# Kernel tuning notes

Hardware: AMD Instinct MI355X
Metric: run time of the kernel (lower is better)

The kernel has to match this reference:

```python
import jax, jax.numpy as jnp
import numpy as np

BZ, T, D, DFF, E, BEAMS = 128, 32, 768, 3072, 8, 2


def setup_inputs() -> dict:
    key = jax.random.key(0)
    ks = jax.random.split(key, 4)
    s = 0.02
    return {
        "x": jax.random.normal(ks[0], (BZ, T, D), jnp.float32),
        "attention_mask": jnp.ones((BZ, T), jnp.float32),
        "Wg": jax.random.normal(ks[1], (D, E), jnp.float32) * s,   # gate Linear(D,E,bias=False)
        "W1": jax.random.normal(ks[2], (E, D, DFF), jnp.float32) * s,
        "b1": jnp.zeros((E, DFF), jnp.float32),
        "W2": jax.random.normal(ks[3], (E, DFF, D), jnp.float32) * s,
        "b2": jnp.zeros((E, D), jnp.float32),
    }


def reference(x, attention_mask, Wg, W1, b1, W2, b2):
    # forward_gate: module builds its own all-ones mask regardless of input mask
    mask = jnp.ones((x.shape[0], x.shape[1]), x.dtype)
    x_avg = (x * mask[..., None]).sum(1) / mask[..., None].sum(1)   # [bz, D]
    prob = jax.nn.softmax(x_avg @ Wg, axis=-1)                       # [bz, E]
    # beam_search (layer_judge='first', pre-route): topk on exp(log(softmax)) == softmax probs
    scores = jnp.exp(jnp.log(prob))
    topv, topi = jax.lax.top_k(scores, BEAMS)                        # [bz, beams]
    beam_scores = topv.reshape(-1)                                   # [bz*beams]
    expert_route = topi.reshape(-1, 1)                                # [bz*beams, 1]
    sel = expert_route[:, -1]
    # replicate x per beam: [bz*beams, T, D]
    x_rep = jnp.broadcast_to(x[:, None], (x.shape[0], BEAMS, x.shape[1], x.shape[2]))
    x_rep = x_rep.reshape(-1, x.shape[1], x.shape[2])
    # per-sample expert FFN dispatch (dense masked loop over the E=8 experts)
    out = jnp.zeros_like(x_rep)
    for e in range(E):
        h = jax.nn.gelu(jnp.einsum('nsd,df->nsf', x_rep, W1[e]) + b1[e], approximate=False)
        ye = jnp.einsum('nsf,fd->nsd', h, W2[e]) + b2[e]
        out = jnp.where((sel == e)[:, None, None], ye, out)
    return (out, beam_scores, expert_route)
```

## Files before the change

### kernel.cpp

```cpp
#include <hip/hip_runtime.h>
#include <cstddef>
#include <cstdint>

#define BZd   128
#define Td    32
#define Dd    768
#define DFFd  3072
#define Ed    8
#define NBEAM 256
#define ROWS_TOT 8192
#define OUT_ELEMS 6291456
#define MAXTILES 72

typedef unsigned short u16;
typedef __attribute__((ext_vector_type(4))) unsigned short ushort4v;
typedef __attribute__((ext_vector_type(8))) short frag_ab;
typedef __attribute__((ext_vector_type(4))) float floatx4;

__device__ __forceinline__ u16 f2bf(float f) {
  unsigned int u = __builtin_bit_cast(unsigned int, f);
  u += 0x7FFFu + ((u >> 16) & 1u);
  return (u16)(u >> 16);
}

__device__ __forceinline__ void async_copy16(u16* lds, const u16* g) {
  __builtin_amdgcn_global_load_lds(
      (const __attribute__((address_space(1))) void*)g,
      (__attribute__((address_space(3))) void*)lds, 16, 0, 0);
}

__device__ __forceinline__ float gelu_fast(float x) {
  float z = 1.5957691216f * (x + 0.044715f * x * x * x);
  return x / (1.0f + __expf(-z));
}

__device__ __forceinline__ void stage8(u16* const (&al)[4], u16* const (&bl)[4],
                                       const u16* (&ag)[4], const u16* (&bg)[4],
                                       int off) {
#pragma unroll
  for (int j = 0; j < 4; j++) {
    async_copy16(al[j] + off, ag[j]);
    async_copy16(bl[j] + off, bg[j]);
    ag[j] += 64;
    bg[j] += 64;
  }
}

__global__ __launch_bounds__(256) void route_kernel(
    const float* __restrict__ x, const float* __restrict__ Wg,
    float* __restrict__ out, int* __restrict__ sel) {
  int b = blockIdx.x;
  int t = threadIdx.x;
  __shared__ float red[256][8];
  float la[8];
#pragma unroll
  for (int e = 0; e < 8; e++) la[e] = 0.f;
  for (int d = t; d < Dd; d += 256) {
    const float* xp = x + (size_t)b * Td * Dd + d;
    float xa = 0.f;
#pragma unroll
    for (int tt = 0; tt < Td; tt++) xa += xp[(size_t)tt * Dd];
    xa *= (1.0f / 32.0f);
#pragma unroll
    for (int e = 0; e < 8; e++) la[e] += xa * Wg[d * 8 + e];
  }
#pragma unroll
  for (int e = 0; e < 8; e++) red[t][e] = la[e];
  __syncthreads();
  for (int s = 128; s > 0; s >>= 1) {
    if (t < s) {
#pragma unroll
      for (int e = 0; e < 8; e++) red[t][e] += red[t + s][e];
    }
    __syncthreads();
  }
  if (t == 0) {
    float lg[8];
#pragma unroll
    for (int e = 0; e < 8; e++) lg[e] = red[0][e];
    float mx = lg[0];
#pragma unroll
    for (int e = 1; e < 8; e++) mx = fmaxf(mx, lg[e]);
    float p[8];
    float sum = 0.f;
#pragma unroll
    for (int e = 0; e < 8; e++) { p[e] = __expf(lg[e] - mx); sum += p[e]; }
    float inv = 1.0f / sum;
#pragma unroll
    for (int e = 0; e < 8; e++) p[e] *= inv;
    int i0 = 0; float v0 = p[0];
#pragma unroll
    for (int e = 1; e < 8; e++) if (p[e] > v0) { v0 = p[e]; i0 = e; }
    int i1 = -1; float v1 = -1.0f;
#pragma unroll
    for (int e = 0; e < 8; e++) if (e != i0 && p[e] > v1) { v1 = p[e]; i1 = e; }
    float* bs = out + OUT_ELEMS;
    float* er = out + OUT_ELEMS + NBEAM;
    bs[2 * b] = v0; bs[2 * b + 1] = v1;
    er[2 * b] = (float)i0; er[2 * b + 1] = (float)i1;
    sel[2 * b] = i0; sel[2 * b + 1] = i1;
  }
}

__global__ __launch_bounds__(256) void bucket_kernel(
    const int* __restrict__ sel, int* __restrict__ perm, int4* __restrict__ tiles) {
  __shared__ int ssel[NBEAM];
  __shared__ int scnt[8];
  __shared__ int soff[8];
  __shared__ int scur[8];
  __shared__ int sperm[NBEAM];
  int t = threadIdx.x;
  ssel[t] = sel[t];
  __syncthreads();
  if (t == 0) {
    for (int e = 0; e < 8; e++) scnt[e] = 0;
    for (int n = 0; n < NBEAM; n++) scnt[ssel[n]]++;
    int o = 0;
    for (int e = 0; e < 8; e++) { soff[e] = o; scur[e] = o; o += scnt[e]; }
    for (int n = 0; n < NBEAM; n++) { int e = ssel[n]; sperm[scur[e]++] = n; }
    int tt = 0;
    for (int e = 0; e < 8; e++) {
      int nr = scnt[e] * 32;
      int base = soff[e] * 32;
      for (int r0 = 0; r0 < nr; r0 += 128) {
        tiles[tt] = make_int4(e, base + r0, min(128, nr - r0), 0);
        tt++;
      }
    }
    for (; tt < MAXTILES; tt++) tiles[tt] = make_int4(-1, 0, 0, 0);
  }
  __syncthreads();
  perm[t] = sperm[t];
}

__global__ __launch_bounds__(256) void convert_x_kernel(
    const float* __restrict__ x, u16* __restrict__ xbf) {
  size_t i = ((size_t)blockIdx.x * 256 + threadIdx.x) * 4;
  float4 v = *(const float4*)(x + i);
  ushort4v pv = {f2bf(v.x), f2bf(v.y), f2bf(v.z), f2bf(v.w)};
  *(ushort4v*)(xbf + i) = pv;
}

__global__ __launch_bounds__(256) void transpose_bf16_kernel(
    const float* __restrict__ in, u16* __restrict__ out, int row0, int col0,
    int ld_in, size_t estr_in, int ld_out, size_t estr_out) {
  __shared__ u16 tile[64][65];
  int e = blockIdx.z;
  int r0 = blockIdx.x * 64, c0 = blockIdx.y * 64;
  int t = threadIdx.x;
  int rr = t >> 4, cc4 = (t & 15) * 4;
  const float* ip = in + (size_t)e * estr_in + (size_t)(row0 + r0) * ld_in + col0 + c0;
#pragma unroll
  for (int i = 0; i < 4; i++) {
    int r = rr + 16 * i;
    float4 v = *(const float4*)(ip + (size_t)r * ld_in + cc4);
    tile[r][cc4 + 0] = f2bf(v.x);
    tile[r][cc4 + 1] = f2bf(v.y);
    tile[r][cc4 + 2] = f2bf(v.z);
    tile[r][cc4 + 3] = f2bf(v.w);
  }
  __syncthreads();
  int ccw = t >> 4, r4 = (t & 15) * 4;
  u16* op = out + (size_t)e * estr_out + (size_t)c0 * ld_out + r0;
#pragma unroll
  for (int i = 0; i < 4; i++) {
    int cc = ccw + 16 * i;
    ushort4v pv = {tile[r4 + 0][cc], tile[r4 + 1][cc], tile[r4 + 2][cc], tile[r4 + 3][cc]};
    *(ushort4v*)(op + (size_t)cc * ld_out + r4) = pv;
  }
}

__global__ __launch_bounds__(256) void gemm1_kernel(
    const u16* __restrict__ xbf, const u16* __restrict__ w1t,
    const float* __restrict__ b1, const int* __restrict__ perm,
    const int4* __restrict__ tiles, u16* __restrict__ h, int f0, int FC) {
  int4 meta = tiles[blockIdx.y];
  int e = meta.x;
  if (e < 0) return;
  int grow0 = meta.y, nrows = meta.z;
  int bx = blockIdx.x;

  __shared__ __align__(16) u16 As[2 * 128 * 64];
  __shared__ __align__(16) u16 Bs[2 * 128 * 64];

  int t = threadIdx.x;
  int l = t & 63, w = t >> 6;
  int wm = w & 1, wn = w >> 1;
  int lrow = l & 15, lquad = l >> 4;

  const u16* ag[4]; const u16* bg[4];
  u16* al[4]; u16* bl[4];
#pragma unroll
  for (int j = 0; j < 4; j++) {
    int s = j * 256 + t;
    int m = s >> 3;
    int koff = (((s & 7) ^ ((m >> 1) & 7))) * 8;
    int bidx = (grow0 >> 5) + (m >> 5);
    bidx = bidx < NBEAM ? bidx : NBEAM - 1;
    int batch = perm[bidx] >> 1;
    ag[j] = xbf + ((size_t)batch * Td + (m & 31)) * Dd + koff;
    bg[j] = w1t + ((size_t)e * FC + bx * 128 + m) * Dd + koff;
    al[j] = As + j * 2048 + w * 512;
    bl[j] = Bs + j * 2048 + w * 512;
  }

  int aoff[2][4], boff[2][4];
#pragma unroll
  for (int hh = 0; hh < 2; hh++)
#pragma unroll
    for (int i = 0; i < 4; i++) {
      int ra = wm * 64 + i * 16 + lrow;
      aoff[hh][i] = ra * 64 + (((lquad + hh * 4) ^ ((ra >> 1) & 7)) * 8);
      int rb = wn * 64 + i * 16 + lrow;
      boff[hh][i] = rb * 64 + (((lquad + hh * 4) ^ ((rb >> 1) & 7)) * 8);
    }

  floatx4 acc[4][4];
#pragma unroll
  for (int mi = 0; mi < 4; mi++)
#pragma unroll
    for (int ni = 0; ni < 4; ni++) acc[mi][ni] = (floatx4){0.f, 0.f, 0.f, 0.f};

  const int nk = Dd / 64;
  stage8(al, bl, ag, bg, 0);

  for (int kt = 0; kt < nk; kt++) {
    const int cur = kt & 1;
    if (kt + 1 < nk) {
      stage8(al, bl, ag, bg, (cur ^ 1) * 8192);
      asm volatile("s_waitcnt vmcnt(8)\n\ts_barrier" ::: "memory");
    } else {
      asm volatile("s_waitcnt vmcnt(0)\n\ts_barrier" ::: "memory");
    }
    const u16* Ab = As + cur * 8192;
    const u16* Bb = Bs + cur * 8192;
#pragma unroll
    for (int hh = 0; hh < 2; hh++) {
      frag_ab af[4], bfr[4];
#pragma unroll
      for (int mi = 0; mi < 4; mi++) af[mi] = *(const frag_ab*)(Ab + aoff[hh][mi]);
#pragma unroll
      for (int ni = 0; ni < 4; ni++) bfr[ni] = *(const frag_ab*)(Bb + boff[hh][ni]);
      __builtin_amdgcn_s_setprio(1);
#pragma unroll
      for (int mi = 0; mi < 4; mi++)
#pragma unroll
        for (int ni = 0; ni < 4; ni++)
          acc[mi][ni] = __builtin_amdgcn_mfma_f32_16x16x32_bf16(bfr[ni], af[mi], acc[mi][ni], 0, 0, 0);
      __builtin_amdgcn_s_setprio(0);
    }
    asm volatile("s_barrier" ::: "memory");
  }

  int f_base = bx * 128;
#pragma unroll
  for (int mi = 0; mi < 4; mi++) {
    int row = wm * 64 + mi * 16 + lrow;
    if (row < nrows) {
      u16* hp = h + (size_t)(grow0 + row) * FC + f_base + wn * 64 + lquad * 4;
      const float* bp = b1 + (size_t)e * DFFd + f0 + f_base + wn * 64 + lquad * 4;
#pragma unroll
      for (int ni = 0; ni < 4; ni++) {
        float4 bias = *(const float4*)(bp + ni * 16);
        ushort4v pv = {f2bf(gelu_fast(acc[mi][ni][0] + bias.x)),
                       f2bf(gelu_fast(acc[mi][ni][1] + bias.y)),
                       f2bf(gelu_fast(acc[mi][ni][2] + bias.z)),
                       f2bf(gelu_fast(acc[mi][ni][3] + bias.w))};
        *(ushort4v*)(hp + ni * 16) = pv;
      }
    }
  }
}

__global__ __launch_bounds__(256) void gemm2_kernel(
    const u16* __restrict__ h, const u16* __restrict__ w2t,
    const float* __restrict__ b2, const int* __restrict__ perm,
    const int4* __restrict__ tiles, float* __restrict__ out,
    int FC, int first) {
  int4 meta = tiles[blockIdx.y];
  int e = meta.x;
  if (e < 0) return;
  int grow0 = meta.y, nrows = meta.z;
  int bx = blockIdx.x;

  __shared__ __align__(16) u16 As[2 * 128 * 64];
  __shared__ __align__(16) u16 Bs[2 * 128 * 64];
  __shared__ int sbeam[4];

  int t = threadIdx.x;
  if (t < 4) {
    int idx = (grow0 >> 5) + t;
    sbeam[t] = perm[idx < NBEAM ? idx : NBEAM - 1];
  }
  __syncthreads();

  int l = t & 63, w = t >> 6;
  int wm = w & 1, wn = w >> 1;
  int lrow = l & 15, lquad = l >> 4;

  const u16* ag[4]; const u16* bg[4];
  u16* al[4]; u16* bl[4];
#pragma unroll
  for (int j = 0; j < 4; j++) {
    int s = j * 256 + t;
    int m = s >> 3;
    int koff = (((s & 7) ^ ((m >> 1) & 7))) * 8;
    int arow = grow0 + m;
    arow = arow < ROWS_TOT ? arow : ROWS_TOT - 1;
    ag[j] = h + (size_t)arow * FC + koff;
    bg[j] = w2t + ((size_t)e * Dd + bx * 128 + m) * FC + koff;
    al[j] = As + j * 2048 + w * 512;
    bl[j] = Bs + j * 2048 + w * 512;
  }

  int aoff[2][4], boff[2][4];
#pragma unroll
  for (int hh = 0; hh < 2; hh++)
#pragma unroll
    for (int i = 0; i < 4; i++) {
      int ra = wm * 64 + i * 16 + lrow;
      aoff[hh][i] = ra * 64 + (((lquad + hh * 4) ^ ((ra >> 1) & 7)) * 8);
      int rb = wn * 64 + i * 16 + lrow;
      boff[hh][i] = rb * 64 + (((lquad + hh * 4) ^ ((rb >> 1) & 7)) * 8);
    }

  floatx4 acc[4][4];
#pragma unroll
  for (int mi = 0; mi < 4; mi++)
#pragma unroll
    for (int ni = 0; ni < 4; ni++) acc[mi][ni] = (floatx4){0.f, 0.f, 0.f, 0.f};

  const int nk = FC / 64;
  stage8(al, bl, ag, bg, 0);

#pragma unroll 2
  for (int kt = 0; kt < nk; kt++) {
    const int cur = kt & 1;
    if (kt + 1 < nk) {
      stage8(al, bl, ag, bg, (cur ^ 1) * 8192);
      asm volatile("s_waitcnt vmcnt(8)\n\ts_barrier" ::: "memory");
    } else {
      asm volatile("s_waitcnt vmcnt(0)\n\ts_barrier" ::: "memory");
    }
    const u16* Ab = As + cur * 8192;
    const u16* Bb = Bs + cur * 8192;
#pragma unroll
    for (int hh = 0; hh < 2; hh++) {
      frag_ab af[4], bfr[4];
#pragma unroll
      for (int mi = 0; mi < 4; mi++) af[mi] = *(const frag_ab*)(Ab + aoff[hh][mi]);
#pragma unroll
      for (int ni = 0; ni < 4; ni++) bfr[ni] = *(const frag_ab*)(Bb + boff[hh][ni]);
      __builtin_amdgcn_s_setprio(1);
#pragma unroll
      for (int mi = 0; mi < 4; mi++)
#pragma unroll
        for (int ni = 0; ni < 4; ni++)
          acc[mi][ni] = __builtin_amdgcn_mfma_f32_16x16x32_bf16(bfr[ni], af[mi], acc[mi][ni], 0, 0, 0);
      __builtin_amdgcn_s_setprio(0);
    }
    asm volatile("s_barrier" ::: "memory");
  }

#pragma unroll
  for (int mi = 0; mi < 4; mi++) {
    int row = wm * 64 + mi * 16 + lrow;
    if (row < nrows) {
      int beam = sbeam[row >> 5];
      float* op = out + ((size_t)beam * Td + (row & 31)) * Dd + bx * 128 + wn * 64 + lquad * 4;
      const float* bp = b2 + (size_t)e * Dd + bx * 128 + wn * 64 + lquad * 4;
#pragma unroll
      for (int ni = 0; ni < 4; ni++) {
        if (first) {
          float4 bias = *(const float4*)(bp + ni * 16);
          float4 v = {acc[mi][ni][0] + bias.x, acc[mi][ni][1] + bias.y,
                      acc[mi][ni][2] + bias.z, acc[mi][ni][3] + bias.w};
          *(float4*)(op + ni * 16) = v;
        } else {
          float4 o = *(float4*)(op + ni * 16);
          o.x += acc[mi][ni][0]; o.y += acc[mi][ni][1];
          o.z += acc[mi][ni][2]; o.w += acc[mi][ni][3];
          *(float4*)(op + ni * 16) = o;
        }
      }
    }
  }
}

extern "C" void kernel_launch(void* const* d_in, const int* in_sizes, int n_in,
                              void* d_out, int out_size, void* d_ws, size_t ws_size,
                              hipStream_t stream) {
  const float* x  = (const float*)d_in[0];
  const float* Wg = (const float*)d_in[2];
  const float* W1 = (const float*)d_in[3];
  const float* b1 = (const float*)d_in[4];
  const float* W2 = (const float*)d_in[5];
  const float* b2 = (const float*)d_in[6];
  float* out = (float*)d_out;

  char* ws = (char*)d_ws;
  int*  sel   = (int*)ws;
  int*  perm  = sel + NBEAM;
  int4* tiles = (int4*)(ws + 4096);

  const size_t xbf_off = 65536;
  const size_t xbf_bytes = (size_t)BZd * Td * Dd * 2;
  int FC = 384;
  if      (xbf_off + xbf_bytes + (size_t)40960 * 3072 <= ws_size) FC = 3072;
  else if (xbf_off + xbf_bytes + (size_t)40960 * 1536 <= ws_size) FC = 1536;
  else if (xbf_off + xbf_bytes + (size_t)40960 * 768  <= ws_size) FC = 768;
  int NC = DFFd / FC;

  u16* xbf = (u16*)(ws + xbf_off);
  u16* w1t = (u16*)(ws + xbf_off + xbf_bytes);
  u16* w2t = w1t + (size_t)Ed * FC * Dd;
  u16* h   = w2t + (size_t)Ed * Dd * FC;

  route_kernel<<<BZd, 256, 0, stream>>>(x, Wg, out, sel);
  bucket_kernel<<<1, 256, 0, stream>>>(sel, perm, tiles);
  convert_x_kernel<<<(BZd * Td * Dd) / 1024, 256, 0, stream>>>(x, xbf);

  for (int c = 0; c < NC; c++) {
    transpose_bf16_kernel<<<dim3(Dd / 64, FC / 64, Ed), 256, 0, stream>>>(
        W1, w1t, 0, c * FC, DFFd, (size_t)Dd * DFFd, Dd, (size_t)FC * Dd);
    transpose_bf16_kernel<<<dim3(FC / 64, Dd / 64, Ed), 256, 0, stream>>>(
        W2, w2t, c * FC, 0, Dd, (size_t)DFFd * Dd, FC, (size_t)Dd * FC);
    gemm1_kernel<<<dim3(FC / 128, MAXTILES), 256, 0, stream>>>(
        xbf, w1t, b1, perm, tiles, h, c * FC, FC);
    gemm2_kernel<<<dim3(Dd / 128, MAXTILES), 256, 0, stream>>>(
        h, w2t, b2, perm, tiles, out, FC, c == 0 ? 1 : 0);
  }
}
```

Before: 379.5 us.

## Enlarge gemm1 tiles to 256x256 with 8 waves and interleaved prefetch

Rewrites the first expert GEMM to use 256-row by 256-column tiles with 512 threads (8 waves, each computing a 128x64 sub-tile), using 128KB of dynamic LDS. A second tile list with 256-row chunks is built in the bucket kernel. Global-to-LDS prefetch of the next K slice is split into four pieces interleaved between MFMA groups instead of issued all at once. The goal is more data reuse per loaded byte and better overlap of loads with compute. The cost is more padding waste on partially filled 256-row tiles, fewer blocks in flight, and higher register pressure from 32 accumulators per thread. The minimum FC fallback is also raised from 384 to 768, so 256-wide column tiles divide it evenly.

```diff
diff --git a/kernel.cpp b/kernel.cpp
--- a/kernel.cpp
+++ b/kernel.cpp
@@ -11,6 +11,7 @@
 #define ROWS_TOT 8192
 #define OUT_ELEMS 6291456
 #define MAXTILES 72
+#define MAXT2    40
 
 typedef unsigned short u16;
 typedef __attribute__((ext_vector_type(4))) unsigned short ushort4v;
@@ -32,18 +33,6 @@
 __device__ __forceinline__ float gelu_fast(float x) {
   float z = 1.5957691216f * (x + 0.044715f * x * x * x);
   return x / (1.0f + __expf(-z));
-}
-
-__device__ __forceinline__ void stage8(u16* const (&al)[4], u16* const (&bl)[4],
-                                       const u16* (&ag)[4], const u16* (&bg)[4],
-                                       int off) {
-#pragma unroll
-  for (int j = 0; j < 4; j++) {
-    async_copy16(al[j] + off, ag[j]);
-    async_copy16(bl[j] + off, bg[j]);
-    ag[j] += 64;
-    bg[j] += 64;
-  }
 }
 
 __global__ __launch_bounds__(256) void route_kernel(
@@ -103,7 +92,8 @@
 }
 
 __global__ __launch_bounds__(256) void bucket_kernel(
-    const int* __restrict__ sel, int* __restrict__ perm, int4* __restrict__ tiles) {
+    const int* __restrict__ sel, int* __restrict__ perm,
+    int4* __restrict__ tiles, int4* __restrict__ tiles2) {
   __shared__ int ssel[NBEAM];
   __shared__ int scnt[8];
   __shared__ int soff[8];
@@ -128,6 +118,16 @@
       }
     }
     for (; tt < MAXTILES; tt++) tiles[tt] = make_int4(-1, 0, 0, 0);
+    int t2 = 0;
+    for (int e = 0; e < 8; e++) {
+      int nr = scnt[e] * 32;
+      int base = soff[e] * 32;
+      for (int r0 = 0; r0 < nr; r0 += 256) {
+        tiles2[t2] = make_int4(e, base + r0, min(256, nr - r0), 0);
+        t2++;
+      }
+    }
+    for (; t2 < MAXT2; t2++) tiles2[t2] = make_int4(-1, 0, 0, 0);
   }
   __syncthreads();
   perm[t] = sperm[t];
@@ -170,95 +170,143 @@
   }
 }
 
-__global__ __launch_bounds__(256) void gemm1_kernel(
+__global__ __launch_bounds__(512, 2) void gemm1_kernel(
     const u16* __restrict__ xbf, const u16* __restrict__ w1t,
     const float* __restrict__ b1, const int* __restrict__ perm,
-    const int4* __restrict__ tiles, u16* __restrict__ h, int f0, int FC) {
-  int4 meta = tiles[blockIdx.y];
+    const int4* __restrict__ tiles2, u16* __restrict__ h, int f0, int FC) {
+  int4 meta = tiles2[blockIdx.y];
   int e = meta.x;
   if (e < 0) return;
   int grow0 = meta.y, nrows = meta.z;
   int bx = blockIdx.x;
 
-  __shared__ __align__(16) u16 As[2 * 128 * 64];
-  __shared__ __align__(16) u16 Bs[2 * 128 * 64];
+  extern __shared__ __align__(16) u16 smem[];
+  u16* As = smem;
+  u16* Bs = smem + 32768;
 
   int t = threadIdx.x;
-  int l = t & 63, w = t >> 6;
-  int wm = w & 1, wn = w >> 1;
+  int l = t & 63;
+  int wid = t >> 6;
+  int wr = wid >> 2;
+  int wc = wid & 3;
   int lrow = l & 15, lquad = l >> 4;
 
   const u16* ag[4]; const u16* bg[4];
-  u16* al[4]; u16* bl[4];
+  int ldst[4];
 #pragma unroll
   for (int j = 0; j < 4; j++) {
-    int s = j * 256 + t;
+    int s = j * 512 + t;
     int m = s >> 3;
-    int koff = (((s & 7) ^ ((m >> 1) & 7))) * 8;
-    int bidx = (grow0 >> 5) + (m >> 5);
-    bidx = bidx < NBEAM ? bidx : NBEAM - 1;
+    int koff = ((s & 7) ^ ((m >> 1) & 7)) * 8;
+    int gr = grow0 + m;
+    int bidx = gr >> 5; bidx = bidx < NBEAM ? bidx : NBEAM - 1;
     int batch = perm[bidx] >> 1;
     ag[j] = xbf + ((size_t)batch * Td + (m & 31)) * Dd + koff;
-    bg[j] = w1t + ((size_t)e * FC + bx * 128 + m) * Dd + koff;
-    al[j] = As + j * 2048 + w * 512;
-    bl[j] = Bs + j * 2048 + w * 512;
-  }
-
-  int aoff[2][4], boff[2][4];
-#pragma unroll
-  for (int hh = 0; hh < 2; hh++)
-#pragma unroll
-    for (int i = 0; i < 4; i++) {
-      int ra = wm * 64 + i * 16 + lrow;
-      aoff[hh][i] = ra * 64 + (((lquad + hh * 4) ^ ((ra >> 1) & 7)) * 8);
-      int rb = wn * 64 + i * 16 + lrow;
-      boff[hh][i] = rb * 64 + (((lquad + hh * 4) ^ ((rb >> 1) & 7)) * 8);
-    }
-
-  floatx4 acc[4][4];
-#pragma unroll
-  for (int mi = 0; mi < 4; mi++)
+    bg[j] = w1t + ((size_t)e * FC + bx * 256 + m) * Dd + koff;
+    ldst[j] = j * 4096 + t * 8;
+  }
+
+  int swz = (lrow >> 1) & 7;
+  int ca0 = (lquad ^ swz) * 8, ca1 = ((lquad + 4) ^ swz) * 8;
+  int abase0 = (wr * 128 + lrow) * 64 + ca0;
+  int abase1 = (wr * 128 + lrow) * 64 + ca1;
+  int bbase0 = (wc * 64 + lrow) * 64 + ca0;
+  int bbase1 = (wc * 64 + lrow) * 64 + ca1;
+
+  floatx4 acc[8][4];
+#pragma unroll
+  for (int mi = 0; mi < 8; mi++)
 #pragma unroll
     for (int ni = 0; ni < 4; ni++) acc[mi][ni] = (floatx4){0.f, 0.f, 0.f, 0.f};
 
   const int nk = Dd / 64;
-  stage8(al, bl, ag, bg, 0);
+
+#pragma unroll
+  for (int j = 0; j < 4; j++) { async_copy16(As + ldst[j], ag[j]); ag[j] += 64; }
+#pragma unroll
+  for (int j = 0; j < 4; j++) { async_copy16(Bs + ldst[j], bg[j]); bg[j] += 64; }
 
   for (int kt = 0; kt < nk; kt++) {
-    const int cur = kt & 1;
-    if (kt + 1 < nk) {
-      stage8(al, bl, ag, bg, (cur ^ 1) * 8192);
-      asm volatile("s_waitcnt vmcnt(8)\n\ts_barrier" ::: "memory");
+    const int b = kt & 1;
+    const u16* Ab = As + b * 16384;
+    const u16* Bb = Bs + b * 16384;
+    const int pd = (b ^ 1) * 16384;
+    const bool pre = (kt + 1 < nk);
+
+    frag_ab af[4], bfr[4];
+
+    if (pre) {
+      async_copy16(As + pd + ldst[0], ag[0]); ag[0] += 64;
+      async_copy16(As + pd + ldst[1], ag[1]); ag[1] += 64;
+      asm volatile("s_waitcnt vmcnt(2)\n\ts_barrier" ::: "memory");
     } else {
       asm volatile("s_waitcnt vmcnt(0)\n\ts_barrier" ::: "memory");
     }
-    const u16* Ab = As + cur * 8192;
-    const u16* Bb = Bs + cur * 8192;
-#pragma unroll
-    for (int hh = 0; hh < 2; hh++) {
-      frag_ab af[4], bfr[4];
-#pragma unroll
-      for (int mi = 0; mi < 4; mi++) af[mi] = *(const frag_ab*)(Ab + aoff[hh][mi]);
-#pragma unroll
-      for (int ni = 0; ni < 4; ni++) bfr[ni] = *(const frag_ab*)(Bb + boff[hh][ni]);
-      __builtin_amdgcn_s_setprio(1);
-#pragma unroll
-      for (int mi = 0; mi < 4; mi++)
-#pragma unroll
-        for (int ni = 0; ni < 4; ni++)
-          acc[mi][ni] = __builtin_amdgcn_mfma_f32_16x16x32_bf16(bfr[ni], af[mi], acc[mi][ni], 0, 0, 0);
-      __builtin_amdgcn_s_setprio(0);
-    }
+#pragma unroll
+    for (int i = 0; i < 4; i++) bfr[i] = *(const frag_ab*)(Bb + bbase0 + i * 1024);
+#pragma unroll
+    for (int i = 0; i < 4; i++) af[i] = *(const frag_ab*)(Ab + abase0 + i * 1024);
+    __builtin_amdgcn_s_setprio(1);
+#pragma unroll
+    for (int mi = 0; mi < 4; mi++)
+#pragma unroll
+      for (int ni = 0; ni < 4; ni++)
+        acc[mi][ni] = __builtin_amdgcn_mfma_f32_16x16x32_bf16(bfr[ni], af[mi], acc[mi][ni], 0, 0, 0);
+    __builtin_amdgcn_s_setprio(0);
+
+    if (pre) {
+      async_copy16(As + pd + ldst[2], ag[2]); ag[2] += 64;
+      async_copy16(As + pd + ldst[3], ag[3]); ag[3] += 64;
+    }
+#pragma unroll
+    for (int i = 0; i < 4; i++) af[i] = *(const frag_ab*)(Ab + abase0 + (i + 4) * 1024);
+    __builtin_amdgcn_s_setprio(1);
+#pragma unroll
+    for (int mi = 0; mi < 4; mi++)
+#pragma unroll
+      for (int ni = 0; ni < 4; ni++)
+        acc[mi + 4][ni] = __builtin_amdgcn_mfma_f32_16x16x32_bf16(bfr[ni], af[mi], acc[mi + 4][ni], 0, 0, 0);
+    __builtin_amdgcn_s_setprio(0);
+
+    if (pre) {
+      async_copy16(Bs + pd + ldst[0], bg[0]); bg[0] += 64;
+      async_copy16(Bs + pd + ldst[1], bg[1]); bg[1] += 64;
+    }
+#pragma unroll
+    for (int i = 0; i < 4; i++) bfr[i] = *(const frag_ab*)(Bb + bbase1 + i * 1024);
+#pragma unroll
+    for (int i = 0; i < 4; i++) af[i] = *(const frag_ab*)(Ab + abase1 + i * 1024);
+    __builtin_amdgcn_s_setprio(1);
+#pragma unroll
+    for (int mi = 0; mi < 4; mi++)
+#pragma unroll
+      for (int ni = 0; ni < 4; ni++)
+        acc[mi][ni] = __builtin_amdgcn_mfma_f32_16x16x32_bf16(bfr[ni], af[mi], acc[mi][ni], 0, 0, 0);
+    __builtin_amdgcn_s_setprio(0);
+
+    if (pre) {
+      async_copy16(Bs + pd + ldst[2], bg[2]); bg[2] += 64;
+      async_copy16(Bs + pd + ldst[3], bg[3]); bg[3] += 64;
+    }
+#pragma unroll
+    for (int i = 0; i < 4; i++) af[i] = *(const frag_ab*)(Ab + abase1 + (i + 4) * 1024);
+    __builtin_amdgcn_s_setprio(1);
+#pragma unroll
+    for (int mi = 0; mi < 4; mi++)
+#pragma unroll
+      for (int ni = 0; ni < 4; ni++)
+        acc[mi + 4][ni] = __builtin_amdgcn_mfma_f32_16x16x32_bf16(bfr[ni], af[mi], acc[mi + 4][ni], 0, 0, 0);
+    __builtin_amdgcn_s_setprio(0);
+
     asm volatile("s_barrier" ::: "memory");
   }
 
-  int f_base = bx * 128;
-#pragma unroll
-  for (int mi = 0; mi < 4; mi++) {
-    int row = wm * 64 + mi * 16 + lrow;
+#pragma unroll
+  for (int mi = 0; mi < 8; mi++) {
+    int row = wr * 128 + mi * 16 + lrow;
     if (row < nrows) {
-      u16* hp = h + (size_t)(grow0 + row) * FC + f_base + wn * 64 + lquad * 4;
-      const float* bp = b1 + (size_t)e * DFFd + f0 + f_base + wn * 64 + lquad * 4;
+      u16* hp = h + (size_t)(grow0 + row) * FC + bx * 256 + wc * 64 + lquad * 4;
+      const float* bp = b1 + (size_t)e * DFFd + f0 + bx * 256 + wc * 64 + lquad * 4;
 #pragma unroll
       for (int ni = 0; ni < 4; ni++) {
         float4 bias = *(const float4*)(bp + ni * 16);
@@ -331,13 +379,23 @@
     for (int ni = 0; ni < 4; ni++) acc[mi][ni] = (floatx4){0.f, 0.f, 0.f, 0.f};
 
   const int nk = FC / 64;
-  stage8(al, bl, ag, bg, 0);
+#pragma unroll
+  for (int j = 0; j < 4; j++) {
+    async_copy16(al[j], ag[j]);
+    async_copy16(bl[j], bg[j]);
+    ag[j] += 64; bg[j] += 64;
+  }
 
 #pragma unroll 2
   for (int kt = 0; kt < nk; kt++) {
     const int cur = kt & 1;
     if (kt + 1 < nk) {
-      stage8(al, bl, ag, bg, (cur ^ 1) * 8192);
+#pragma unroll
+      for (int j = 0; j < 4; j++) {
+        async_copy16(al[j] + (cur ^ 1) * 8192, ag[j]);
+        async_copy16(bl[j] + (cur ^ 1) * 8192, bg[j]);
+        ag[j] += 64; bg[j] += 64;
+      }
       asm volatile("s_waitcnt vmcnt(8)\n\ts_barrier" ::: "memory");
     } else {
       asm volatile("s_waitcnt vmcnt(0)\n\ts_barrier" ::: "memory");
@@ -399,16 +457,16 @@
   float* out = (float*)d_out;
 
   char* ws = (char*)d_ws;
-  int*  sel   = (int*)ws;
-  int*  perm  = sel + NBEAM;
-  int4* tiles = (int4*)(ws + 4096);
+  int*  sel    = (int*)ws;
+  int*  perm   = sel + NBEAM;
+  int4* tiles  = (int4*)(ws + 4096);
+  int4* tiles2 = (int4*)(ws + 6144);
 
   const size_t xbf_off = 65536;
   const size_t xbf_bytes = (size_t)BZd * Td * Dd * 2;
-  int FC = 384;
+  int FC = 768;
   if      (xbf_off + xbf_bytes + (size_t)40960 * 3072 <= ws_size) FC = 3072;
   else if (xbf_off + xbf_bytes + (size_t)40960 * 1536 <= ws_size) FC = 1536;
-  else if (xbf_off + xbf_bytes + (size_t)40960 * 768  <= ws_size) FC = 768;
   int NC = DFFd / FC;
 
   u16* xbf = (u16*)(ws + xbf_off);
@@ -416,8 +474,15 @@
   u16* w2t = w1t + (size_t)Ed * FC * Dd;
   u16* h   = w2t + (size_t)Ed * Dd * FC;
 
+  static bool attr_done = false;
+  if (!attr_done) {
+    hipFuncSetAttribute(reinterpret_cast<const void*>(gemm1_kernel),
+                        hipFuncAttributeMaxDynamicSharedMemorySize, 131072);
+    attr_done = true;
+  }
+
   route_kernel<<<BZd, 256, 0, stream>>>(x, Wg, out, sel);
-  bucket_kernel<<<1, 256, 0, stream>>>(sel, perm, tiles);
+  bucket_kernel<<<1, 256, 0, stream>>>(sel, perm, tiles, tiles2);
   convert_x_kernel<<<(BZd * Td * Dd) / 1024, 256, 0, stream>>>(x, xbf);
 
   for (int c = 0; c < NC; c++) {
@@ -425,8 +490,8 @@
         W1, w1t, 0, c * FC, DFFd, (size_t)Dd * DFFd, Dd, (size_t)FC * Dd);
     transpose_bf16_kernel<<<dim3(FC / 64, Dd / 64, Ed), 256, 0, stream>>>(
         W2, w2t, c * FC, 0, Dd, (size_t)DFFd * Dd, FC, (size_t)Dd * FC);
-    gemm1_kernel<<<dim3(FC / 128, MAXTILES), 256, 0, stream>>>(
-        xbf, w1t, b1, perm, tiles, h, c * FC, FC);
+    gemm1_kernel<<<dim3(FC / 256, MAXT2), 512, 131072, stream>>>(
+        xbf, w1t, b1, perm, tiles2, h, c * FC, FC);
     gemm2_kernel<<<dim3(Dd / 128, MAXTILES), 256, 0, stream>>>(
         h, w2t, b2, perm, tiles, out, FC, c == 0 ? 1 : 0);
   }
```

New measurement: 366.4 us. -3.5%, faster.
